# Kernel optimization log

Hardware: AMD Instinct MI355X
Metric: run time of the kernel (lower is better)

## Reference

```python
import jax, jax.numpy as jnp
import numpy as np

# Module hyperparameters (from init_kwargs)
P = 96                 # num_of_patches
W = 1536.0             # input width
H = 1536.0             # input height
XPS = W / P            # x patch size = 16
YPS = H / P            # y patch size = 16
PROB_THR = 0.9
IOU_THR = 0.5
N = P * P              # total candidate boxes


def setup_inputs() -> dict:
    key = jax.random.key(0)
    # x: [5, P, P] -> channel 0 = probability, 1..4 = (x, y, w, h) in [0,1)
    x = jax.random.uniform(key, (5, P, P), dtype=jnp.float32)
    return {"x": x}


def _pairwise_iou(b):
    # b: [N, 4] xyxy
    x1, y1, x2, y2 = b[:, 0], b[:, 1], b[:, 2], b[:, 3]
    area = (x2 - x1) * (y2 - y1)                       # [N]
    ix1 = jnp.maximum(x1[:, None], x1[None, :])
    iy1 = jnp.maximum(y1[:, None], y1[None, :])
    ix2 = jnp.minimum(x2[:, None], x2[None, :])
    iy2 = jnp.minimum(y2[:, None], y2[None, :])
    inter = jnp.clip(ix2 - ix1, 0.0) * jnp.clip(iy2 - iy1, 0.0)
    union = area[:, None] + area[None, :] - inter
    return jnp.where(union > 0, inter / union, 0.0)    # [N, N]


def _forward(x):
    # --- scale_batch_bbx_xywh, applied densely (invalid entries are masked later) ---
    p = x[0]
    ii = jnp.arange(P, dtype=x.dtype)[:, None]   # row index i
    jj = jnp.arange(P, dtype=x.dtype)[None, :]   # col index j
    bx = x[1] * XPS + ii * XPS
    by = x[2] * YPS + jj * YPS
    bw = x[3] * W
    bh = x[4] * H
    bbx = jnp.stack([p, bx, by, bw, bh], axis=0).reshape(5, N).T   # [N, 5] (p, x, y, w, h)

    # --- remove_low_probability_bbx: fixed-shape validity mask instead of filtering ---
    scores = bbx[:, 0]
    valid = scores > PROB_THR

    # --- convert_batch_to_xyxy + round ---
    x1 = jnp.round(bbx[:, 1])
    y1 = jnp.round(bbx[:, 2])
    x2 = jnp.round(bbx[:, 3] + bbx[:, 1])
    y2 = jnp.round(bbx[:, 4] + bbx[:, 2])

    # --- greedy NMS (torchvision semantics): sort by score desc, suppress by IoU ---
    sort_key = jnp.where(valid, scores, -jnp.inf)
    order = jnp.argsort(-sort_key)
    boxes = jnp.stack([x1, y1, x2, y2], axis=1)[order]   # [N, 4] sorted
    sc = scores[order]
    v = valid[order]
    iou = _pairwise_iou(boxes)                           # [N, N]

    def body(kept, i):
        suppressed = jnp.any(kept & (iou[i] > IOU_THR))
        ki = v[i] & ~suppressed
        return kept.at[i].set(ki), ki

    _, keeps = jax.lax.scan(body, jnp.zeros((N,), bool), jnp.arange(N))

    # --- cat([scores, bbx]) then convert_batch_to_xywh on kept rows ---
    out = jnp.stack(
        [sc, boxes[:, 0], boxes[:, 1], boxes[:, 2] - boxes[:, 0], boxes[:, 3] - boxes[:, 1]],
        axis=1,
    )  # [N, 5] = (score, x, y, w, h), score-descending order like nms output
    out = jnp.where(keeps[:, None], out, 0.0)
    return out, keeps


def reference(x):
    # Returns (out [N,5], keep_mask [N]); rows with keep_mask=False are zeroed.
    # This is the fixed-shape equivalent of the variable-length torch output.
    return _forward(x)
```

## Files before the change

kernel.cpp:

```cpp
#include <hip/hip_runtime.h>

#define PP 96
#define NB (PP*PP)
#define NCH (NB/64)
#define PROB_THR 0.9f
#define FAST_CAP 1024
#define LSTRIDE 1034

typedef unsigned long long u64;
typedef unsigned int u32;

__device__ __forceinline__ void decode_core(int n, float xv, float yv, float wv, float hv,
                                            float& X1, float& Y1, float& X2, float& Y2)
{
    int i = n / PP;
    int j = n - i * PP;
    float bx = __fadd_rn(__fmul_rn(xv, 16.0f), (float)i * 16.0f);
    float by = __fadd_rn(__fmul_rn(yv, 16.0f), (float)j * 16.0f);
    float bw = __fmul_rn(wv, 1536.0f);
    float bh = __fmul_rn(hv, 1536.0f);
    X1 = rintf(bx);
    Y1 = rintf(by);
    X2 = rintf(__fadd_rn(bw, bx));
    Y2 = rintf(__fadd_rn(bh, by));
}

__device__ __forceinline__ void decode_box(const float* __restrict__ x, int n,
                                           float& X1, float& Y1, float& X2, float& Y2)
{
    decode_core(n, x[NB + n], x[2 * NB + n], x[3 * NB + n], x[4 * NB + n], X1, Y1, X2, Y2);
}

__device__ __forceinline__ int iou_hit_nodiv(float ix1, float iy1, float ix2, float iy2, float iar,
                                             float jx1, float jy1, float jx2, float jy2, float jar)
{
    float xx1 = fmaxf(ix1, jx1), yy1 = fmaxf(iy1, jy1);
    float xx2 = fminf(ix2, jx2), yy2 = fminf(iy2, jy2);
    float iw = fmaxf(__fsub_rn(xx2, xx1), 0.0f);
    float ih = fmaxf(__fsub_rn(yy2, yy1), 0.0f);
    float inter = __fmul_rn(iw, ih);
    float uni = __fsub_rn(__fadd_rn(iar, jar), inter);
    return (uni > 0.0f && __fadd_rn(inter, inter) > uni) ? 1 : 0;
}

__device__ __forceinline__ int iou_hit_div(float ix1, float iy1, float ix2, float iy2, float iar,
                                           float jx1, float jy1, float jx2, float jy2, float jar)
{
    float xx1 = fmaxf(ix1, jx1), yy1 = fmaxf(iy1, jy1);
    float xx2 = fminf(ix2, jx2), yy2 = fminf(iy2, jy2);
    float iw = fmaxf(__fsub_rn(xx2, xx1), 0.0f);
    float ih = fmaxf(__fsub_rn(yy2, yy1), 0.0f);
    float inter = __fmul_rn(iw, ih);
    float uni = __fsub_rn(__fadd_rn(iar, jar), inter);
    return (uni > 0.0f && __fdiv_rn(inter, uni) > 0.5f) ? 1 : 0;
}

__global__ void __launch_bounds__(256) k_front(
    const float* __restrict__ x,
    float* __restrict__ gss, float4* __restrict__ gbox,
    u64* __restrict__ skeys, int* __restrict__ counter,
    u64* __restrict__ adjT, int ws_ok)
{
    __shared__ u64 lmask[NCH];
    __shared__ int pc[NCH], loff[NCH];
    __shared__ int sM;
    __shared__ u64 kdb[FAST_CAP];
    __shared__ float4 lb[FAST_CAP];
    __shared__ float la[FAST_CAP];

    const int tid = threadIdx.x;
    const int lane = tid & 63;
    const int wv = tid >> 6;
    const int b = blockIdx.x;

    #pragma unroll
    for (int g = 0; g < 36; g += 6) {
        float sv[6];
        #pragma unroll
        for (int u = 0; u < 6; ++u)
            sv[u] = x[((wv * 36 + g + u) << 6) + lane];
        #pragma unroll
        for (int u = 0; u < 6; ++u) {
            u64 m = __ballot(sv[u] > PROB_THR);
            if (lane == 0) lmask[wv * 36 + g + u] = m;
        }
    }
    __syncthreads();
    if (tid < NCH) pc[tid] = __popcll(lmask[tid]);
    __syncthreads();
    if (tid < 64) {
        int acc = 0;
        for (int seg = 0; seg < 3; ++seg) {
            int c = (seg << 6) + lane;
            int pv = (c < NCH) ? pc[c] : 0;
            int v = pv;
            #pragma unroll
            for (int off = 1; off < 64; off <<= 1) {
                int u = __shfl_up(v, off);
                if (lane >= off) v += u;
            }
            if (c < NCH) loff[c] = acc + v - pv;
            acc += __shfl(v, 63);
        }
        if (lane == 0) sM = acc;
    }
    __syncthreads();
    const int M = sM;
    const bool fast = (M <= FAST_CAP) && ws_ok;
    if (b == 0 && tid == 0) counter[0] = M;

    if (!fast) {
        if (b == 0) {
            for (int c = wv; c < NCH; c += 4) {
                float s = x[(c << 6) + lane];
                u64 m = lmask[c];
                if ((m >> lane) & 1ull) {
                    int pos = loff[c] + __popcll(m & ((1ull << lane) - 1ull));
                    int n = (c << 6) + lane;
                    skeys[pos] = ((u64)__float_as_uint(s) << 32) | (u64)(NB - 1 - n);
                }
            }
        }
        return;
    }
    if (b != 0 && (b << 4) >= M) return;

    for (int c = wv; c < NCH; c += 4) {
        float s = x[(c << 6) + lane];
        u64 m = lmask[c];
        if ((m >> lane) & 1ull) {
            int pos = loff[c] + __popcll(m & ((1ull << lane) - 1ull));
            int n = (c << 6) + lane;
            kdb[pos] = ((u64)__float_as_uint(s) << 32) | (u64)(NB - 1 - n);
        }
    }
    for (int q = M + tid; q < FAST_CAP; q += 256) kdb[q] = 0ull;
    __syncthreads();

    u64 k0v[4]; int rkv[4]; int n0v[4];
    float xvv[4], yvv[4], wvv[4], hvv[4];
    #pragma unroll
    for (int g = 0; g < 4; ++g) {
        k0v[g] = kdb[(g << 8) + tid];
        rkv[g] = 0;
        n0v[g] = NB - 1 - (int)(k0v[g] & 0xFFFFFFFFull);
        xvv[g] = x[NB + n0v[g]];
        yvv[g] = x[2 * NB + n0v[g]];
        wvv[g] = x[3 * NB + n0v[g]];
        hvv[g] = x[4 * NB + n0v[g]];
    }
    const int nck = (M + 63) >> 6;
    for (int ch = 0; ch < nck; ++ch) {
        u64 kq = kdb[(ch << 6) + lane];
        u32 qlo = (u32)kq, qhi = (u32)(kq >> 32);
        #pragma unroll
        for (int i = 0; i < 64; ++i) {
            u32 blo = (u32)__builtin_amdgcn_readlane((int)qlo, i);
            u32 bhi = (u32)__builtin_amdgcn_readlane((int)qhi, i);
            u64 kb = ((u64)bhi << 32) | (u64)blo;
            #pragma unroll
            for (int g = 0; g < 4; ++g)
                rkv[g] += (kb > k0v[g]) ? 1 : 0;
        }
    }

    #pragma unroll
    for (int g = 0; g < 4; ++g) {
        int cand = (g << 8) + tid;
        if (cand < M) {
            float X1, Y1, X2, Y2;
            decode_core(n0v[g], xvv[g], yvv[g], wvv[g], hvv[g], X1, Y1, X2, Y2);
            float4 bb = make_float4(X1, Y1, X2, Y2);
            int rk = rkv[g];
            lb[rk] = bb;
            la[rk] = __fmul_rn(__fsub_rn(X2, X1), __fsub_rn(Y2, Y1));
            if (b == 0) {
                gbox[rk] = bb;
                gss[rk] = __uint_as_float((u32)(k0v[g] >> 32));
            }
        }
    }
    __syncthreads();

    const int W = (M + 63) >> 6;
    #pragma unroll
    for (int r = 0; r < 4; ++r) {
        int i = (b << 4) + (r << 2) + wv;
        if (i >= M) break;
        float4 bi = lb[i];
        float iar = la[i];
        for (int kk = 0; kk < W; ++kk) {
            int j = (kk << 6) + lane;
            float4 bj = lb[j & (FAST_CAP - 1)];
            float jar = la[j & (FAST_CAP - 1)];
            int hit = (j < M) && iou_hit_nodiv(bi.x, bi.y, bi.z, bi.w, iar,
                                               bj.x, bj.y, bj.z, bj.w, jar);
            u64 mm = __ballot(hit);
            if (lane == 0) adjT[((size_t)kk << 10) + i] = mm;
        }
    }
}

__global__ void __launch_bounds__(256) k_sweep(
    const float* __restrict__ x, float* __restrict__ out,
    float* __restrict__ gss, float4* __restrict__ gbox,
    const u64* __restrict__ skeys, const int* __restrict__ counter,
    const u64* __restrict__ adjT, int ws_ok)
{
    __shared__ __align__(16) u64 Lds[16 * LSTRIDE];
    __shared__ u64 keepw[NCH];

    const int tid = threadIdx.x, lane = tid & 63;

    {
        float4 z4 = make_float4(0.f, 0.f, 0.f, 0.f);
        for (int q = tid; q < 13824; q += 256)
            ((float4*)out)[q] = z4;
    }

    int M = counter[0]; if (M > NB) M = NB;
    const int W = (M + 63) >> 6;
    const bool fast = (M <= FAST_CAP) && ws_ok;

    if (fast) {
        const int npair = W << 9;
        const ulonglong2* gp = (const ulonglong2*)adjT;
        for (int r = 0; r < 4; ++r) {
            int fb = (r << 11) + tid;
            ulonglong2 v[8];
            #pragma unroll
            for (int u = 0; u < 8; ++u) {
                int f = fb + (u << 8);
                v[u] = (f < npair) ? gp[f] : make_ulonglong2(0ull, 0ull);
            }
            #pragma unroll
            for (int u = 0; u < 8; ++u) {
                int f = fb + (u << 8);
                if (f < npair) {
                    int w = f >> 9, r2 = f & 511;
                    ((ulonglong2*)Lds)[w * (LSTRIDE >> 1) + r2] = v[u];
                }
            }
        }
        __syncthreads();

        if (tid < 64) {
            const int wl = (lane < W) ? lane : 0;
            u32 supl = 0u, suph = 0u, dl = 0u, dh = 0u;
            u64 mykw = 0ull;
            const int nrb = (M + 31) >> 5;
            for (int rb = 0; rb < nrb; ++rb) {
                const int c = rb >> 1;
                const int base = rb << 5;
                const ulonglong2* crow = (const ulonglong2*)(Lds + (size_t)c * LSTRIDE + base);
                const ulonglong2* rrow = (const ulonglong2*)(Lds + (size_t)wl * LSTRIDE + base);
                u64 colb[32], rowb[32];
                #pragma unroll
                for (int q = 0; q < 16; ++q) {
                    ulonglong2 t2 = crow[q];
                    colb[2 * q] = t2.x; colb[2 * q + 1] = t2.y;
                }
                #pragma unroll
                for (int q = 0; q < 16; ++q) {
                    ulonglong2 t2 = rrow[q];
                    rowb[2 * q] = t2.x; rowb[2 * q + 1] = t2.y;
                }
                if (!(rb & 1)) {
                    if (rb == 0) { dl = 0u; dh = 0u; }
                    else { dl = (u32)__shfl((int)supl, c); dh = (u32)__shfl((int)suph, c); }
                    int rem = M - (c << 6);
                    if (rem < 64) {
                        if (rem >= 32) dh |= 0xFFFFFFFFu << (rem - 32);
                        else { dh = 0xFFFFFFFFu; dl |= 0xFFFFFFFFu << rem; }
                    }
                }
                u32 kw = 0u;
                if (!(rb & 1)) {
                    #pragma unroll
                    for (int t = 0; t < 32; ++t) {
                        u32 bbit = (dl >> t) & 1u;
                        u32 m = bbit - 1u;
                        dl |= (u32)colb[t] & m;
                        dh |= (u32)(colb[t] >> 32) & m;
                        kw |= m & (1u << t);
                    }
                } else {
                    #pragma unroll
                    for (int t = 0; t < 32; ++t) {
                        u32 bbit = (dh >> t) & 1u;
                        u32 m = bbit - 1u;
                        dl |= (u32)colb[t] & m;
                        dh |= (u32)(colb[t] >> 32) & m;
                        kw |= m & (1u << t);
                    }
                }
                #pragma unroll
                for (int t = 0; t < 32; ++t) {
                    u32 m = 0u - ((kw >> t) & 1u);
                    supl |= (u32)rowb[t] & m;
                    suph |= (u32)(rowb[t] >> 32) & m;
                }
                mykw |= (lane == c) ? ((u64)kw << ((rb & 1) << 5)) : 0ull;
            }
            keepw[lane] = mykw;
        }
    } else {
        for (int t = tid; t < M; t += 256) {
            u64 key = skeys[t];
            int r = 0;
            for (int q = 0; q < M; ++q) r += (skeys[q] > key) ? 1 : 0;
            int n = NB - 1 - (int)(key & 0xFFFFFFFFull);
            float X1, Y1, X2, Y2;
            decode_box(x, n, X1, Y1, X2, Y2);
            gbox[r] = make_float4(X1, Y1, X2, Y2);
            gss[r] = __uint_as_float((u32)(key >> 32));
        }
        __threadfence();
        __syncthreads();
        if (tid < 64) {
            u64 kbs[3] = {0ull, 0ull, 0ull};
            for (int i = 0; i < M; ++i) {
                float4 bi = gbox[i];
                float iar = __fmul_rn(__fsub_rn(bi.z, bi.x), __fsub_rn(bi.w, bi.y));
                int hit = 0;
                int nk = (i > lane) ? ((i - lane + 63) >> 6) : 0;
                for (int w = 0; w < 3 && !hit; ++w) {
                    int klim = nk - (w << 6);
                    if (klim <= 0) break;
                    u64 bits = kbs[w];
                    if (klim < 64) bits &= ((1ull << klim) - 1ull);
                    while (bits) {
                        int kk2 = __builtin_ctzll(bits);
                        bits &= bits - 1ull;
                        int jj = lane + (((w << 6) + kk2) << 6);
                        float4 bj = gbox[jj];
                        float jar = __fmul_rn(__fsub_rn(bj.z, bj.x), __fsub_rn(bj.w, bj.y));
                        if (iou_hit_div(bi.x, bi.y, bi.z, bi.w, iar,
                                        bj.x, bj.y, bj.z, bj.w, jar)) { hit = 1; break; }
                    }
                }
                int suppressed = __any(hit);
                if (!suppressed && lane == (i & 63)) kbs[(i >> 6) >> 6] |= 1ull << ((i >> 6) & 63);
            }
            int NWrd = (M + 63) >> 6;
            for (int wd = 0; wd < NWrd; ++wd) {
                u64 bit = (kbs[wd >> 6] >> (wd & 63)) & 1ull;
                u64 word = __ballot(bit != 0);
                if (lane == 0 && wd < NCH) keepw[wd] = word;
            }
        }
    }
    __syncthreads();

    for (int i = tid; i < M; i += 256) {
        if ((keepw[i >> 6] >> (i & 63)) & 1ull) {
            float4 bb = gbox[i];
            out[i * 5 + 0] = gss[i];
            out[i * 5 + 1] = bb.x;
            out[i * 5 + 2] = bb.y;
            out[i * 5 + 3] = __fsub_rn(bb.z, bb.x);
            out[i * 5 + 4] = __fsub_rn(bb.w, bb.y);
            out[5 * NB + i] = 1.0f;
        }
    }
}

extern "C" void kernel_launch(void* const* d_in, const int* in_sizes, int n_in,
                              void* d_out, int out_size, void* d_ws, size_t ws_size,
                              hipStream_t stream) {
    const float* x = (const float*)d_in[0];
    float* out = (float*)d_out;

    char* ws = (char*)d_ws;
    int* counter = (int*)ws;
    float*  gss  = (float*)(ws + 16);
    float4* gbox = (float4*)(ws + 16 + (size_t)4 * NB);
    u64*    adjT = (u64*)(ws + 16 + (size_t)4 * NB + (size_t)16 * NB);
    u64*    skeys = (u64*)((char*)adjT + (size_t)16384 * 8);
    const size_t NEEDED = 16 + (size_t)4 * NB + (size_t)16 * NB
                        + (size_t)16384 * 8 + (size_t)8 * NB;
    int ws_ok = (ws_size >= NEEDED) ? 1 : 0;

    k_front<<<64, 256, 0, stream>>>(x, gss, gbox, skeys, counter, adjT, ws_ok);
    k_sweep<<<1, 256, 0, stream>>>(x, out, gss, gbox, skeys, counter, adjT, ws_ok);
}
```

Before: 120.1 us.

## Replace rank-counting sort with in-LDS bitonic sort and halve front grid

```diff
diff --git a/kernel.cpp b/kernel.cpp
--- a/kernel.cpp
+++ b/kernel.cpp
@@ -123,7 +123,7 @@
         }
         return;
     }
-    if (b != 0 && (b << 4) >= M) return;
+    if (b != 0 && (b << 5) >= M) return;
 
     for (int c = wv; c < NCH; c += 4) {
         float s = x[(c << 6) + lane];
@@ -137,46 +137,42 @@
     for (int q = M + tid; q < FAST_CAP; q += 256) kdb[q] = 0ull;
     __syncthreads();
 
-    u64 k0v[4]; int rkv[4]; int n0v[4];
-    float xvv[4], yvv[4], wvv[4], hvv[4];
+    #pragma unroll 1
+    for (int k = 2; k <= FAST_CAP; k <<= 1) {
+        #pragma unroll 1
+        for (int j = k >> 1; j > 0; j >>= 1) {
+            #pragma unroll
+            for (int e0 = 0; e0 < FAST_CAP; e0 += 256) {
+                int e = e0 + tid;
+                int p = e ^ j;
+                if (p > e) {
+                    u64 a = kdb[e], c2 = kdb[p];
+                    bool desc = ((e & k) == 0);
+                    if (desc ? (a < c2) : (a > c2)) { kdb[e] = c2; kdb[p] = a; }
+                }
+            }
+            __syncthreads();
+        }
+    }
+
     #pragma unroll
     for (int g = 0; g < 4; ++g) {
-        k0v[g] = kdb[(g << 8) + tid];
-        rkv[g] = 0;
-        n0v[g] = NB - 1 - (int)(k0v[g] & 0xFFFFFFFFull);
-        xvv[g] = x[NB + n0v[g]];
-        yvv[g] = x[2 * NB + n0v[g]];
-        wvv[g] = x[3 * NB + n0v[g]];
-        hvv[g] = x[4 * NB + n0v[g]];
-    }
-    const int nck = (M + 63) >> 6;
-    for (int ch = 0; ch < nck; ++ch) {
-        u64 kq = kdb[(ch << 6) + lane];
-        u32 qlo = (u32)kq, qhi = (u32)(kq >> 32);
-        #pragma unroll
-        for (int i = 0; i < 64; ++i) {
-            u32 blo = (u32)__builtin_amdgcn_readlane((int)qlo, i);
-            u32 bhi = (u32)__builtin_amdgcn_readlane((int)qhi, i);
-            u64 kb = ((u64)bhi << 32) | (u64)blo;
-            #pragma unroll
-            for (int g = 0; g < 4; ++g)
-                rkv[g] += (kb > k0v[g]) ? 1 : 0;
-        }
-    }
-
-    #pragma unroll
-    for (int g = 0; g < 4; ++g) {
-        int cand = (g << 8) + tid;
-        if (cand < M) {
+        int slot = (g << 8) + tid;
+        u64 key = kdb[slot];
+        int n0 = NB - 1 - (int)(key & 0xFFFFFFFFull);
+        float xv = x[NB + n0];
+        float yv = x[2 * NB + n0];
+        float wvv = x[3 * NB + n0];
+        float hvv = x[4 * NB + n0];
+        if (slot < M) {
             float X1, Y1, X2, Y2;
-            decode_core(n0v[g], xvv[g], yvv[g], wvv[g], hvv[g], X1, Y1, X2, Y2);
+            decode_core(n0, xv, yv, wvv, hvv, X1, Y1, X2, Y2);
             float4 bb = make_float4(X1, Y1, X2, Y2);
-            int rk = rkv[g];
-            lb[rk] = bb;
-            la[rk] = __fmul_rn(__fsub_rn(X2, X1), __fsub_rn(Y2, Y1));
+            lb[slot] = bb;
+            la[slot] = __fmul_rn(__fsub_rn(X2, X1), __fsub_rn(Y2, Y1));
             if (b == 0) {
-                gbox[rk] = bb;
-                gss[rk] = __uint_as_float((u32)(k0v[g] >> 32));
+                gbox[slot] = bb;
+                gss[slot] = __uint_as_float((u32)(key >> 32));
             }
         }
     }
@@ -184,8 +180,8 @@
 
     const int W = (M + 63) >> 6;
     #pragma unroll
-    for (int r = 0; r < 4; ++r) {
-        int i = (b << 4) + (r << 2) + wv;
+    for (int r = 0; r < 8; ++r) {
+        int i = (b << 5) + (r << 2) + wv;
         if (i >= M) break;
         float4 bi = lb[i];
         float iar = la[i];
@@ -381,6 +377,6 @@
                         + (size_t)16384 * 8 + (size_t)8 * NB;
     int ws_ok = (ws_size >= NEEDED) ? 1 : 0;
 
-    k_front<<<64, 256, 0, stream>>>(x, gss, gbox, skeys, counter, adjT, ws_ok);
+    k_front<<<32, 256, 0, stream>>>(x, gss, gbox, skeys, counter, adjT, ws_ok);
     k_sweep<<<1, 256, 0, stream>>>(x, out, gss, gbox, skeys, counter, adjT, ws_ok);
 }
```

Result: slower. 138.7 us (+15.5%).
